# Kernel optimization log

Hardware: AMD Instinct MI355X
Metric: run time of the kernel (lower is better)

Reference implementation:

```python
import jax, jax.numpy as jnp
import numpy as np

N_FREQS = 6  # PositionEmbedding default used by LISA


def setup_inputs() -> dict:
    key = jax.random.key(0)
    ks = jax.random.split(key, 8)
    B, L, N, D, H = 8, 32768, 2048, 64, 256
    in_dim = 1 * (2 * N_FREQS + 1) + 3 * D  # 13 + 192 = 205

    def w(k, i, o):
        return jax.random.normal(k, (i, o), jnp.float32) * (1.0 / np.sqrt(i))

    return {
        "coord": jax.random.uniform(ks[0], (B, L, 1), jnp.float32),
        "latent": jax.random.normal(ks[1], (B, N, D), jnp.float32),
        "W0": w(ks[2], in_dim, H), "b0": jnp.zeros((H,), jnp.float32),
        "W1": w(ks[3], H, H), "b1": jnp.zeros((H,), jnp.float32),
        "W2": w(ks[4], H, H), "b2": jnp.zeros((H,), jnp.float32),
        "W3": w(ks[5], H, H), "b3": jnp.zeros((H,), jnp.float32),
        "W4": w(ks[6], H, 1), "b4": jnp.zeros((1,), jnp.float32),
    }


def reference(coord, latent, W0, b0, W1, b1, W2, b2, W3, b3, W4, b4):
    B, N, D = latent.shape
    # feat_unfold: concat shifted-prev / self / shifted-next along channels
    feat = jnp.swapaxes(latent, 1, 2)                                   # [B, D, N]
    feat_prev = jnp.concatenate([feat[:, :, :1], feat[:, :, :-1]], axis=2)
    feat_next = jnp.concatenate([feat[:, :, 1:], feat[:, :, -1:]], axis=2)
    feat = jnp.concatenate([feat_prev, feat, feat_next], axis=1)        # [B, 3D, N]

    # grid_sample(bilinear, padding_mode='border', align_corners=False) on a
    # 1-row image: y coordinate 0 hits row 0 exactly, so only x interpolates.
    # torch mapping: ix = ((gx + 1) * W - 1) / 2 with gx = coord*2 - 1
    ix = coord[..., 0] * N - 0.5                                        # [B, L]
    x0 = jnp.floor(ix)
    t = ix - x0                                                         # lerp weight
    i0 = jnp.clip(x0.astype(jnp.int32), 0, N - 1)                       # border clamp
    i1 = jnp.clip(x0.astype(jnp.int32) + 1, 0, N - 1)
    f0 = jnp.take_along_axis(feat, i0[:, None, :], axis=2)              # [B, 3D, L]
    f1 = jnp.take_along_axis(feat, i1[:, None, :], axis=2)
    sampled = (1.0 - t)[:, None, :] * f0 + t[:, None, :] * f1
    sampled = jnp.swapaxes(sampled, 1, 2)                               # [B, L, 3D]

    # positional encoding: [x, sin(f x), cos(f x) for f in 1,2,4,8,16,32]
    freqs = 2.0 ** jnp.arange(N_FREQS, dtype=jnp.float32)
    ang = coord * freqs                                                 # [B, L, 6]
    pe = jnp.stack([jnp.sin(ang), jnp.cos(ang)], axis=-1)
    pe = pe.reshape(ang.shape[0], ang.shape[1], 2 * N_FREQS)            # [B, L, 12]

    inp = jnp.concatenate([coord, pe, sampled], axis=-1)                # [B, L, 205]

    h = jax.nn.relu(inp @ W0 + b0)
    h = jax.nn.relu(h @ W1 + b1)
    h = jax.nn.relu(h @ W2 + b2)
    h = jax.nn.relu(h @ W3 + b3)
    return h @ W4 + b4                                                  # [B, L, 1]
```

## Files before the change

### kernel.cpp

```cpp
#include <hip/hip_runtime.h>
#include <hip/hip_bf16.h>

typedef unsigned short ushort_t;
typedef unsigned int uint_t;
typedef __attribute__((ext_vector_type(8))) short short8;
typedef __attribute__((ext_vector_type(4))) float float4v;
typedef __attribute__((ext_vector_type(4))) uint_t uint4v;

#define NLAT 2048
#define DLAT 64

#define PW_BASE 128
#define PW0_OFF 0
#define PW1_OFF 57344
#define PW2_OFF 122880
#define PW3_OFF 188416

__device__ __forceinline__ float b2f(ushort_t u) {
  union { uint_t i; float f; } v; v.i = ((uint_t)u) << 16; return v.f;
}
__device__ __forceinline__ ushort_t f2b(float f) {
  uint_t x = __float_as_uint(f);
  uint_t r = (x + 0x7fffu + ((x >> 16) & 1u)) >> 16;
  return (ushort_t)r;
}
__device__ __forceinline__ uint_t pack2(float lo, float hi) {
  float2 t; t.x = lo; t.y = hi;
  union { __hip_bfloat162 h; uint_t u; } cv;
  cv.h = __float22bfloat162_rn(t);
  return cv.u;
}
__device__ __forceinline__ int imin(int a, int b) { return a < b ? a : b; }
__device__ __forceinline__ int imax(int a, int b) { return a > b ? a : b; }

__device__ __forceinline__ float ldv(const float* p, long i)    { return p[i]; }
__device__ __forceinline__ float ldv(const ushort_t* p, long i) { return b2f(p[i]); }
__device__ __forceinline__ void stv(float* p, long i, float v)    { p[i] = v; }
__device__ __forceinline__ void stv(ushort_t* p, long i, float v) { p[i] = f2b(v); }

__device__ __forceinline__ float4 load4f(const float* p) { return *(const float4*)p; }
__device__ __forceinline__ float4 load4f(const ushort_t* p) {
  uint2 u = *(const uint2*)p;
  float4 r;
  r.x = b2f((ushort_t)(u.x & 0xffffu)); r.y = b2f((ushort_t)(u.x >> 16));
  r.z = b2f((ushort_t)(u.y & 0xffffu)); r.w = b2f((ushort_t)(u.y >> 16));
  return r;
}

__device__ __forceinline__ void async_copy16(const ushort_t* g, ushort_t* l) {
  __builtin_amdgcn_global_load_lds(
      (const __attribute__((address_space(1))) void*)g,
      (__attribute__((address_space(3))) void*)l, 16, 0, 0);
}

template <int KT>
__device__ __forceinline__ void stage_q_t(ushort_t* dst, const ushort_t* src, int tid) {
#pragma unroll
  for (int r = 0; r < KT; ++r) {
    int i = tid + (r << 8);
    async_copy16(src + (size_t)i * 8, dst + (size_t)i * 8);
  }
}
__device__ __forceinline__ void stage_gi(int gi, ushort_t* dst,
                                         const ushort_t* __restrict__ pw, int tid) {
  int layer = gi >> 2, q = gi & 3;
  if (layer == 0) {
    stage_q_t<7>(dst, pw + PW0_OFF + q * 7 * 2048, tid);
  } else {
    int loff = (layer == 1) ? PW1_OFF : (layer == 2) ? PW2_OFF : PW3_OFF;
    stage_q_t<8>(dst, pw + loff + q * 8 * 2048, tid);
  }
}

__global__ void detect_mode(const ushort_t* __restrict__ lat, int* __restrict__ flag) {
  if (threadIdx.x == 0) *flag = 0;
  __syncthreads();
  int big = 0;
  for (int i = threadIdx.x; i < 1024; i += 64) {
    float v = b2f(lat[i]);
    if (!(fabsf(v) < 1e5f)) big = 1;
  }
  if (__any(big) && threadIdx.x == 0) *flag = 1;
}

template <typename TI>
__global__ void pack_w_t(const TI* __restrict__ W0, const TI* __restrict__ W1,
                         const TI* __restrict__ W2, const TI* __restrict__ W3,
                         ushort_t* __restrict__ pw, const int* __restrict__ flag, int want)
{
  if (*flag != want) return;
  int g = blockIdx.x * blockDim.x + threadIdx.x;
  if (g >= 31 * 1024) return;
  int lane = g & 63, q = lane >> 4;
  int mt   = (g >> 6) & 15;
  int ktg  = g >> 10;
  const TI* W; ushort_t* dst; int kt, KT; bool isw0 = false;
  if (ktg < 7)       { W = W0; dst = pw + PW0_OFF; kt = ktg;      KT = 7; isw0 = true; }
  else if (ktg < 15) { W = W1; dst = pw + PW1_OFF; kt = ktg - 7;  KT = 8; }
  else if (ktg < 23) { W = W2; dst = pw + PW2_OFF; kt = ktg - 15; KT = 8; }
  else               { W = W3; dst = pw + PW3_OFF; kt = ktg - 23; KT = 8; }
  int col = mt * 16 + (lane & 15);
  uint_t words[4];
#pragma unroll
  for (int h = 0; h < 4; ++h) {
    ushort_t vv[2];
#pragma unroll
    for (int e = 0; e < 2; ++e) {
      int j = 2 * h + e;
      int f = 32 * kt + 16 * (j >> 2) + 4 * q + (j & 3);
      int row = f;
      if (isw0) row = (f < 192) ? (13 + f) : (f == 192 ? 0 : (f <= 204 ? f - 192 : -1));
      vv[e] = (row >= 0) ? f2b(ldv(W, (long)row * 256 + col)) : (ushort_t)0;
    }
    words[h] = (uint_t)vv[0] | ((uint_t)vv[1] << 16);
  }
  uint4 o; o.x = words[0]; o.y = words[1]; o.z = words[2]; o.w = words[3];
  *(uint4*)(dst + ((size_t)(mt * KT + kt) * 64 + lane) * 8) = o;
}

template <int KT>
__device__ __forceinline__ void run_layer(int base, float4v (&acc)[16][2],
                                          const uint4v (&hu)[8][2],
                                          ushort_t (*wbuf)[16384],
                                          const ushort_t* __restrict__ pw,
                                          int tid, int lane)
{
#pragma unroll
  for (int qq = 0; qq < 4; ++qq) {
    const int gi = base + qq;
    if (gi + 1 < 16) stage_gi(gi + 1, wbuf[(gi + 1) & 1], pw, tid);
    const ushort_t* buf = wbuf[gi & 1];
#pragma unroll
    for (int m = 0; m < 4; ++m) {
      acc[qq * 4 + m][0] = (float4v){0.f, 0.f, 0.f, 0.f};
      acc[qq * 4 + m][1] = (float4v){0.f, 0.f, 0.f, 0.f};
    }
    short8 aL[2], aH[2];
    aL[0] = *(const short8*)&buf[((size_t)(0 * KT + 0) * 64 + lane) * 8];
    aL[1] = *(const short8*)&buf[((size_t)(1 * KT + 0) * 64 + lane) * 8];
#pragma unroll
    for (int kt = 0; kt < KT; ++kt) {
      aH[0] = *(const short8*)&buf[((size_t)(2 * KT + kt) * 64 + lane) * 8];
      aH[1] = *(const short8*)&buf[((size_t)(3 * KT + kt) * 64 + lane) * 8];
      short8 b0 = __builtin_bit_cast(short8, hu[kt][0]);
      short8 b1 = __builtin_bit_cast(short8, hu[kt][1]);
      acc[qq * 4 + 0][0] = __builtin_amdgcn_mfma_f32_16x16x32_bf16(aL[0], b0, acc[qq * 4 + 0][0], 0, 0, 0);
      acc[qq * 4 + 0][1] = __builtin_amdgcn_mfma_f32_16x16x32_bf16(aL[0], b1, acc[qq * 4 + 0][1], 0, 0, 0);
      acc[qq * 4 + 1][0] = __builtin_amdgcn_mfma_f32_16x16x32_bf16(aL[1], b0, acc[qq * 4 + 1][0], 0, 0, 0);
      acc[qq * 4 + 1][1] = __builtin_amdgcn_mfma_f32_16x16x32_bf16(aL[1], b1, acc[qq * 4 + 1][1], 0, 0, 0);
      if (kt + 1 < KT) {
        aL[0] = *(const short8*)&buf[((size_t)(0 * KT + kt + 1) * 64 + lane) * 8];
        aL[1] = *(const short8*)&buf[((size_t)(1 * KT + kt + 1) * 64 + lane) * 8];
      }
      acc[qq * 4 + 2][0] = __builtin_amdgcn_mfma_f32_16x16x32_bf16(aH[0], b0, acc[qq * 4 + 2][0], 0, 0, 0);
      acc[qq * 4 + 2][1] = __builtin_amdgcn_mfma_f32_16x16x32_bf16(aH[0], b1, acc[qq * 4 + 2][1], 0, 0, 0);
      acc[qq * 4 + 3][0] = __builtin_amdgcn_mfma_f32_16x16x32_bf16(aH[1], b0, acc[qq * 4 + 3][0], 0, 0, 0);
      acc[qq * 4 + 3][1] = __builtin_amdgcn_mfma_f32_16x16x32_bf16(aH[1], b1, acc[qq * 4 + 3][1], 0, 0, 0);
    }
    __syncthreads();
  }
}

__device__ __forceinline__ void convert_layer(float4v (&acc)[16][2], uint4v (&hu)[8][2],
                                              const float* bwl, int q)
{
#pragma unroll
  for (int mt = 0; mt < 16; ++mt) {
    float4 b4 = *(const float4*)&bwl[mt * 16 + 4 * q];
#pragma unroll
    for (int g = 0; g < 2; ++g) {
      float v0 = fmaxf(acc[mt][g][0] + b4.x, 0.f);
      float v1 = fmaxf(acc[mt][g][1] + b4.y, 0.f);
      float v2 = fmaxf(acc[mt][g][2] + b4.z, 0.f);
      float v3 = fmaxf(acc[mt][g][3] + b4.w, 0.f);
      hu[mt >> 1][g][(mt & 1) * 2 + 0] = pack2(v0, v1);
      hu[mt >> 1][g][(mt & 1) * 2 + 1] = pack2(v2, v3);
    }
  }
}

template <typename TI>
__global__ __launch_bounds__(256, 2) void lisa_fused_t(
    const TI* __restrict__ coord, const TI* __restrict__ latent,
    const TI* __restrict__ bias0, const TI* __restrict__ bias1,
    const TI* __restrict__ bias2, const TI* __restrict__ bias3,
    const TI* __restrict__ W4,    const TI* __restrict__ b4,
    const ushort_t* __restrict__ pw, TI* __restrict__ out,
    const int* __restrict__ flag, int want)
{
  if (*flag != want) return;
  __shared__ __align__(16) ushort_t wbuf[2][16384];
  __shared__ __align__(16) float bw[4 * 256 + 256 + 1];

  const int tid  = threadIdx.x;
  const int lane = tid & 63, q = lane >> 4, m15 = lane & 15;
  const int wv   = tid >> 6;
  const long pbase = (long)blockIdx.x * 128 + wv * 32 + m15;

  stage_gi(0, wbuf[0], pw, tid);
  for (int i = tid; i < 1281; i += 256) {
    float v;
    if (i < 256)       v = ldv(bias0, i);
    else if (i < 512)  v = ldv(bias1, i - 256);
    else if (i < 768)  v = ldv(bias2, i - 512);
    else if (i < 1024) v = ldv(bias3, i - 768);
    else if (i < 1280) v = ldv(W4, i - 1024);
    else               v = ldv(b4, 0);
    bw[i] = v;
  }

  uint4v hu[8][2];
#pragma unroll
  for (int g = 0; g < 2; ++g) {
    long p = pbase + g * 16;
    float c   = ldv(coord, p);
    float ixv = c * 2048.0f - 0.5f;
    float x0f = floorf(ixv);
    float t   = ixv - x0f;
    int   x0  = (int)x0f;
    int   i0  = imin(imax(x0, 0), NLAT - 1);
    int   i1  = imin(imax(x0 + 1, 0), NLAT - 1);
    float w0 = 1.0f - t, w1 = t;
    int rows0[3] = { imax(i0 - 1, 0), i0, imin(i0 + 1, NLAT - 1) };
    int rows1[3] = { imax(i1 - 1, 0), i1, imin(i1 + 1, NLAT - 1) };
    const TI* lat = latent + (size_t)(p >> 15) * (NLAT * DLAT);
#pragma unroll
    for (int tb = 0; tb < 12; ++tb) {
      int region = tb >> 2;
      int d0 = 16 * (tb & 3) + 4 * q;
      float4 a = load4f(lat + (long)rows0[region] * DLAT + d0);
      float4 b = load4f(lat + (long)rows1[region] * DLAT + d0);
      hu[tb >> 1][g][(tb & 1) * 2 + 0] = pack2(w0 * a.x + w1 * b.x, w0 * a.y + w1 * b.y);
      hu[tb >> 1][g][(tb & 1) * 2 + 1] = pack2(w0 * a.z + w1 * b.z, w0 * a.w + w1 * b.w);
    }
    float pv[4];
#pragma unroll
    for (int s = 0; s < 4; ++s) {
      int f = 192 + 4 * q + s;
      float v = 0.0f;
      if (f == 192) v = c;
      else if (f <= 204) {
        int i = f - 193;
        float fr = (float)(1 << (i >> 1));
        float ang = c * fr;
        v = (i & 1) ? __cosf(ang) : __sinf(ang);
      }
      pv[s] = v;
    }
    hu[6][g][0] = pack2(pv[0], pv[1]);
    hu[6][g][1] = pack2(pv[2], pv[3]);
    hu[6][g][2] = 0; hu[6][g][3] = 0;
  }
  __syncthreads();

  float4v acc[16][2];

  run_layer<7>( 0, acc, hu, wbuf, pw, tid, lane);
  convert_layer(acc, hu, bw + 0 * 256, q);
  run_layer<8>( 4, acc, hu, wbuf, pw, tid, lane);
  convert_layer(acc, hu, bw + 1 * 256, q);
  run_layer<8>( 8, acc, hu, wbuf, pw, tid, lane);
  convert_layer(acc, hu, bw + 2 * 256, q);
  run_layer<8>(12, acc, hu, wbuf, pw, tid, lane);

  float partial0 = 0.f, partial1 = 0.f;
#pragma unroll
  for (int mt = 0; mt < 16; ++mt) {
    float4 b3v = *(const float4*)&bw[3 * 256 + mt * 16 + 4 * q];
    float4 w4v = *(const float4*)&bw[1024 + mt * 16 + 4 * q];
    float v;
    v = fmaxf(acc[mt][0][0] + b3v.x, 0.f); partial0 += v * w4v.x;
    v = fmaxf(acc[mt][0][1] + b3v.y, 0.f); partial0 += v * w4v.y;
    v = fmaxf(acc[mt][0][2] + b3v.z, 0.f); partial0 += v * w4v.z;
    v = fmaxf(acc[mt][0][3] + b3v.w, 0.f); partial0 += v * w4v.w;
    v = fmaxf(acc[mt][1][0] + b3v.x, 0.f); partial1 += v * w4v.x;
    v = fmaxf(acc[mt][1][1] + b3v.y, 0.f); partial1 += v * w4v.y;
    v = fmaxf(acc[mt][1][2] + b3v.z, 0.f); partial1 += v * w4v.z;
    v = fmaxf(acc[mt][1][3] + b3v.w, 0.f); partial1 += v * w4v.w;
  }
  partial0 += __shfl_xor(partial0, 16, 64);
  partial0 += __shfl_xor(partial0, 32, 64);
  partial1 += __shfl_xor(partial1, 16, 64);
  partial1 += __shfl_xor(partial1, 32, 64);
  if (lane < 16) {
    float bb = bw[1280];
    stv(out, pbase,      partial0 + bb);
    stv(out, pbase + 16, partial1 + bb);
  }
}

extern "C" void kernel_launch(void* const* d_in, const int* in_sizes, int n_in,
                              void* d_out, int out_size, void* d_ws, size_t ws_size,
                              hipStream_t stream) {
  int* flag = (int*)d_ws;
  ushort_t* pw = (ushort_t*)d_ws + PW_BASE;

  detect_mode<<<1, 64, 0, stream>>>((const ushort_t*)d_in[1], flag);

  pack_w_t<float><<<62, 512, 0, stream>>>(
      (const float*)d_in[2], (const float*)d_in[4], (const float*)d_in[6],
      (const float*)d_in[8], pw, flag, 1);
  lisa_fused_t<float><<<2048, 256, 0, stream>>>(
      (const float*)d_in[0], (const float*)d_in[1],
      (const float*)d_in[3], (const float*)d_in[5], (const float*)d_in[7],
      (const float*)d_in[9], (const float*)d_in[10], (const float*)d_in[11],
      pw, (float*)d_out, flag, 1);

  pack_w_t<ushort_t><<<62, 512, 0, stream>>>(
      (const ushort_t*)d_in[2], (const ushort_t*)d_in[4], (const ushort_t*)d_in[6],
      (const ushort_t*)d_in[8], pw, flag, 0);
  lisa_fused_t<ushort_t><<<2048, 256, 0, stream>>>(
      (const ushort_t*)d_in[0], (const ushort_t*)d_in[1],
      (const ushort_t*)d_in[3], (const ushort_t*)d_in[5], (const ushort_t*)d_in[7],
      (const ushort_t*)d_in[9], (const ushort_t*)d_in[10], (const ushort_t*)d_in[11],
      pw, (ushort_t*)d_out, flag, 0);
}
```

Before: 225.1 us.

## Split output neurons across waves and share activations through LDS

Each wave previously computed all 256 output neurons for its own 32 points, staging every weight quarter into LDS with double-buffered async copies. Now each wave owns 64 output neurons for all 128 points of the block. The weights are read directly from global memory (cached) into registers, and activations are exchanged between layers through an LDS buffer, with block barriers around each conversion. The final layer needs a cross-wave reduction of partial sums through LDS. This removes the weight staging into LDS and its barriers, but adds activation LDS traffic and relies on L1/L2 serving the repeated global weight reads.

```diff
diff --git a/kernel.cpp b/kernel.cpp
--- a/kernel.cpp
+++ b/kernel.cpp
@@ -45,31 +45,6 @@
   r.x = b2f((ushort_t)(u.x & 0xffffu)); r.y = b2f((ushort_t)(u.x >> 16));
   r.z = b2f((ushort_t)(u.y & 0xffffu)); r.w = b2f((ushort_t)(u.y >> 16));
   return r;
-}
-
-__device__ __forceinline__ void async_copy16(const ushort_t* g, ushort_t* l) {
-  __builtin_amdgcn_global_load_lds(
-      (const __attribute__((address_space(1))) void*)g,
-      (__attribute__((address_space(3))) void*)l, 16, 0, 0);
-}
-
-template <int KT>
-__device__ __forceinline__ void stage_q_t(ushort_t* dst, const ushort_t* src, int tid) {
-#pragma unroll
-  for (int r = 0; r < KT; ++r) {
-    int i = tid + (r << 8);
-    async_copy16(src + (size_t)i * 8, dst + (size_t)i * 8);
-  }
-}
-__device__ __forceinline__ void stage_gi(int gi, ushort_t* dst,
-                                         const ushort_t* __restrict__ pw, int tid) {
-  int layer = gi >> 2, q = gi & 3;
-  if (layer == 0) {
-    stage_q_t<7>(dst, pw + PW0_OFF + q * 7 * 2048, tid);
-  } else {
-    int loff = (layer == 1) ? PW1_OFF : (layer == 2) ? PW2_OFF : PW3_OFF;
-    stage_q_t<8>(dst, pw + loff + q * 8 * 2048, tid);
-  }
 }
 
 __global__ void detect_mode(const ushort_t* __restrict__ lat, int* __restrict__ flag) {
@@ -119,64 +94,68 @@
 }
 
 template <int KT>
-__device__ __forceinline__ void run_layer(int base, float4v (&acc)[16][2],
-                                          const uint4v (&hu)[8][2],
-                                          ushort_t (*wbuf)[16384],
-                                          const ushort_t* __restrict__ pw,
-                                          int tid, int lane)
+__device__ __forceinline__ void run_layer_new(const ushort_t* __restrict__ pwl,
+                                              float4v (&acc)[4][8],
+                                              const ushort_t* __restrict__ act,
+                                              int lane, int wv)
 {
 #pragma unroll
-  for (int qq = 0; qq < 4; ++qq) {
-    const int gi = base + qq;
-    if (gi + 1 < 16) stage_gi(gi + 1, wbuf[(gi + 1) & 1], pw, tid);
-    const ushort_t* buf = wbuf[gi & 1];
-#pragma unroll
-    for (int m = 0; m < 4; ++m) {
-      acc[qq * 4 + m][0] = (float4v){0.f, 0.f, 0.f, 0.f};
-      acc[qq * 4 + m][1] = (float4v){0.f, 0.f, 0.f, 0.f};
-    }
-    short8 aL[2], aH[2];
-    aL[0] = *(const short8*)&buf[((size_t)(0 * KT + 0) * 64 + lane) * 8];
-    aL[1] = *(const short8*)&buf[((size_t)(1 * KT + 0) * 64 + lane) * 8];
-#pragma unroll
-    for (int kt = 0; kt < KT; ++kt) {
-      aH[0] = *(const short8*)&buf[((size_t)(2 * KT + kt) * 64 + lane) * 8];
-      aH[1] = *(const short8*)&buf[((size_t)(3 * KT + kt) * 64 + lane) * 8];
-      short8 b0 = __builtin_bit_cast(short8, hu[kt][0]);
-      short8 b1 = __builtin_bit_cast(short8, hu[kt][1]);
-      acc[qq * 4 + 0][0] = __builtin_amdgcn_mfma_f32_16x16x32_bf16(aL[0], b0, acc[qq * 4 + 0][0], 0, 0, 0);
-      acc[qq * 4 + 0][1] = __builtin_amdgcn_mfma_f32_16x16x32_bf16(aL[0], b1, acc[qq * 4 + 0][1], 0, 0, 0);
-      acc[qq * 4 + 1][0] = __builtin_amdgcn_mfma_f32_16x16x32_bf16(aL[1], b0, acc[qq * 4 + 1][0], 0, 0, 0);
-      acc[qq * 4 + 1][1] = __builtin_amdgcn_mfma_f32_16x16x32_bf16(aL[1], b1, acc[qq * 4 + 1][1], 0, 0, 0);
-      if (kt + 1 < KT) {
-        aL[0] = *(const short8*)&buf[((size_t)(0 * KT + kt + 1) * 64 + lane) * 8];
-        aL[1] = *(const short8*)&buf[((size_t)(1 * KT + kt + 1) * 64 + lane) * 8];
-      }
-      acc[qq * 4 + 2][0] = __builtin_amdgcn_mfma_f32_16x16x32_bf16(aH[0], b0, acc[qq * 4 + 2][0], 0, 0, 0);
-      acc[qq * 4 + 2][1] = __builtin_amdgcn_mfma_f32_16x16x32_bf16(aH[0], b1, acc[qq * 4 + 2][1], 0, 0, 0);
-      acc[qq * 4 + 3][0] = __builtin_amdgcn_mfma_f32_16x16x32_bf16(aH[1], b0, acc[qq * 4 + 3][0], 0, 0, 0);
-      acc[qq * 4 + 3][1] = __builtin_amdgcn_mfma_f32_16x16x32_bf16(aH[1], b1, acc[qq * 4 + 3][1], 0, 0, 0);
-    }
-    __syncthreads();
-  }
-}
-
-__device__ __forceinline__ void convert_layer(float4v (&acc)[16][2], uint4v (&hu)[8][2],
-                                              const float* bwl, int q)
+  for (int m = 0; m < 4; ++m)
+#pragma unroll
+    for (int p = 0; p < 8; ++p)
+      acc[m][p] = (float4v){0.f, 0.f, 0.f, 0.f};
+
+  const ushort_t* abase = pwl + (((size_t)(4 * wv) * KT) * 64 + lane) * 8;
+
+  short8 A0[4], A1[4];
+#pragma unroll
+  for (int m = 0; m < 4; ++m)
+    A0[m] = *(const short8*)(abase + (size_t)(m * KT) * 512);
+
+#pragma unroll
+  for (int kt = 0; kt < KT; ++kt) {
+    short8 (&Ac)[4] = (kt & 1) ? A1 : A0;
+    short8 (&An)[4] = (kt & 1) ? A0 : A1;
+    if (kt + 1 < KT) {
+#pragma unroll
+      for (int m = 0; m < 4; ++m)
+        An[m] = *(const short8*)(abase + (size_t)(m * KT + kt + 1) * 512);
+    }
+#pragma unroll
+    for (int p = 0; p < 8; ++p) {
+      short8 B = *(const short8*)&act[((size_t)(p * 8 + kt) * 64 + lane) * 8];
+      acc[0][p] = __builtin_amdgcn_mfma_f32_16x16x32_bf16(Ac[0], B, acc[0][p], 0, 0, 0);
+      acc[1][p] = __builtin_amdgcn_mfma_f32_16x16x32_bf16(Ac[1], B, acc[1][p], 0, 0, 0);
+      acc[2][p] = __builtin_amdgcn_mfma_f32_16x16x32_bf16(Ac[2], B, acc[2][p], 0, 0, 0);
+      acc[3][p] = __builtin_amdgcn_mfma_f32_16x16x32_bf16(Ac[3], B, acc[3][p], 0, 0, 0);
+    }
+  }
+}
+
+__device__ __forceinline__ void convert_store(float4v (&acc)[4][8],
+                                              ushort_t* __restrict__ act,
+                                              const float* __restrict__ bwl,
+                                              int lane, int wv, int q)
 {
-#pragma unroll
-  for (int mt = 0; mt < 16; ++mt) {
-    float4 b4 = *(const float4*)&bwl[mt * 16 + 4 * q];
-#pragma unroll
-    for (int g = 0; g < 2; ++g) {
-      float v0 = fmaxf(acc[mt][g][0] + b4.x, 0.f);
-      float v1 = fmaxf(acc[mt][g][1] + b4.y, 0.f);
-      float v2 = fmaxf(acc[mt][g][2] + b4.z, 0.f);
-      float v3 = fmaxf(acc[mt][g][3] + b4.w, 0.f);
-      hu[mt >> 1][g][(mt & 1) * 2 + 0] = pack2(v0, v1);
-      hu[mt >> 1][g][(mt & 1) * 2 + 1] = pack2(v2, v3);
-    }
-  }
+  __syncthreads();
+#pragma unroll
+  for (int p2 = 0; p2 < 2; ++p2) {
+    const float4 bE = *(const float4*)&bwl[wv * 64 + p2 * 32 + 4 * q];
+    const float4 bO = *(const float4*)&bwl[wv * 64 + p2 * 32 + 16 + 4 * q];
+    const int kt = 2 * wv + p2;
+#pragma unroll
+    for (int p = 0; p < 8; ++p) {
+      const float4v& aE = acc[2 * p2][p];
+      const float4v& aO = acc[2 * p2 + 1][p];
+      uint4 o;
+      o.x = pack2(fmaxf(aE[0] + bE.x, 0.f), fmaxf(aE[1] + bE.y, 0.f));
+      o.y = pack2(fmaxf(aE[2] + bE.z, 0.f), fmaxf(aE[3] + bE.w, 0.f));
+      o.z = pack2(fmaxf(aO[0] + bO.x, 0.f), fmaxf(aO[1] + bO.y, 0.f));
+      o.w = pack2(fmaxf(aO[2] + bO.z, 0.f), fmaxf(aO[3] + bO.w, 0.f));
+      *(uint4*)&act[((size_t)(p * 8 + kt) * 64 + lane) * 8] = o;
+    }
+  }
+  __syncthreads();
 }
 
 template <typename TI>
@@ -189,7 +168,7 @@
     const int* __restrict__ flag, int want)
 {
   if (*flag != want) return;
-  __shared__ __align__(16) ushort_t wbuf[2][16384];
+  __shared__ __align__(16) ushort_t act[8 * 8 * 64 * 8];
   __shared__ __align__(16) float bw[4 * 256 + 256 + 1];
 
   const int tid  = threadIdx.x;
@@ -197,7 +176,6 @@
   const int wv   = tid >> 6;
   const long pbase = (long)blockIdx.x * 128 + wv * 32 + m15;
 
-  stage_gi(0, wbuf[0], pw, tid);
   for (int i = tid; i < 1281; i += 256) {
     float v;
     if (i < 256)       v = ldv(bias0, i);
@@ -209,7 +187,7 @@
     bw[i] = v;
   }
 
-  uint4v hu[8][2];
+  uint4v hu[7][2];
 #pragma unroll
   for (int g = 0; g < 2; ++g) {
     long p = pbase + g * 16;
@@ -250,42 +228,57 @@
     hu[6][g][0] = pack2(pv[0], pv[1]);
     hu[6][g][1] = pack2(pv[2], pv[3]);
     hu[6][g][2] = 0; hu[6][g][3] = 0;
-  }
-  __syncthreads();
-
-  float4v acc[16][2];
-
-  run_layer<7>( 0, acc, hu, wbuf, pw, tid, lane);
-  convert_layer(acc, hu, bw + 0 * 256, q);
-  run_layer<8>( 4, acc, hu, wbuf, pw, tid, lane);
-  convert_layer(acc, hu, bw + 1 * 256, q);
-  run_layer<8>( 8, acc, hu, wbuf, pw, tid, lane);
-  convert_layer(acc, hu, bw + 2 * 256, q);
-  run_layer<8>(12, acc, hu, wbuf, pw, tid, lane);
-
-  float partial0 = 0.f, partial1 = 0.f;
-#pragma unroll
-  for (int mt = 0; mt < 16; ++mt) {
-    float4 b3v = *(const float4*)&bw[3 * 256 + mt * 16 + 4 * q];
-    float4 w4v = *(const float4*)&bw[1024 + mt * 16 + 4 * q];
-    float v;
-    v = fmaxf(acc[mt][0][0] + b3v.x, 0.f); partial0 += v * w4v.x;
-    v = fmaxf(acc[mt][0][1] + b3v.y, 0.f); partial0 += v * w4v.y;
-    v = fmaxf(acc[mt][0][2] + b3v.z, 0.f); partial0 += v * w4v.z;
-    v = fmaxf(acc[mt][0][3] + b3v.w, 0.f); partial0 += v * w4v.w;
-    v = fmaxf(acc[mt][1][0] + b3v.x, 0.f); partial1 += v * w4v.x;
-    v = fmaxf(acc[mt][1][1] + b3v.y, 0.f); partial1 += v * w4v.y;
-    v = fmaxf(acc[mt][1][2] + b3v.z, 0.f); partial1 += v * w4v.z;
-    v = fmaxf(acc[mt][1][3] + b3v.w, 0.f); partial1 += v * w4v.w;
-  }
-  partial0 += __shfl_xor(partial0, 16, 64);
-  partial0 += __shfl_xor(partial0, 32, 64);
-  partial1 += __shfl_xor(partial1, 16, 64);
-  partial1 += __shfl_xor(partial1, 32, 64);
+
+    const int pt = 2 * wv + g;
+#pragma unroll
+    for (int kt = 0; kt < 7; ++kt)
+      *(uint4v*)&act[((size_t)(pt * 8 + kt) * 64 + lane) * 8] = hu[kt][g];
+  }
+  __syncthreads();
+
+  float4v acc[4][8];
+
+  run_layer_new<7>(pw + PW0_OFF, acc, act, lane, wv);
+  convert_store(acc, act, bw + 0 * 256, lane, wv, q);
+  run_layer_new<8>(pw + PW1_OFF, acc, act, lane, wv);
+  convert_store(acc, act, bw + 1 * 256, lane, wv, q);
+  run_layer_new<8>(pw + PW2_OFF, acc, act, lane, wv);
+  convert_store(acc, act, bw + 2 * 256, lane, wv, q);
+  run_layer_new<8>(pw + PW3_OFF, acc, act, lane, wv);
+
+  __syncthreads();
+
+  float psum[8];
+#pragma unroll
+  for (int p = 0; p < 8; ++p) psum[p] = 0.f;
+#pragma unroll
+  for (int m = 0; m < 4; ++m) {
+    const float4 b3v = *(const float4*)&bw[3 * 256 + wv * 64 + m * 16 + 4 * q];
+    const float4 w4v = *(const float4*)&bw[1024 + wv * 64 + m * 16 + 4 * q];
+#pragma unroll
+    for (int p = 0; p < 8; ++p) {
+      float v;
+      v = fmaxf(acc[m][p][0] + b3v.x, 0.f); psum[p] += v * w4v.x;
+      v = fmaxf(acc[m][p][1] + b3v.y, 0.f); psum[p] += v * w4v.y;
+      v = fmaxf(acc[m][p][2] + b3v.z, 0.f); psum[p] += v * w4v.z;
+      v = fmaxf(acc[m][p][3] + b3v.w, 0.f); psum[p] += v * w4v.w;
+    }
+  }
+#pragma unroll
+  for (int p = 0; p < 8; ++p) {
+    psum[p] += __shfl_xor(psum[p], 16, 64);
+    psum[p] += __shfl_xor(psum[p], 32, 64);
+  }
+  float* part = (float*)act;
   if (lane < 16) {
-    float bb = bw[1280];
-    stv(out, pbase,      partial0 + bb);
-    stv(out, pbase + 16, partial1 + bb);
+#pragma unroll
+    for (int p = 0; p < 8; ++p) part[wv * 128 + p * 16 + lane] = psum[p];
+  }
+  __syncthreads();
+  if (tid < 128) {
+    float s = part[tid] + part[128 + tid] + part[256 + tid] + part[384 + tid]
+            + bw[1280];
+    stv(out, (long)blockIdx.x * 128 + tid, s);
   }
 }
 
```

Result: no change. 221.5 us (-1.6%).
